# Kernel optimization log

Hardware: AMD Instinct MI355X
Metric: run time of the kernel (lower is better)

## Reference

```python
import math
import jax, jax.numpy as jnp
import numpy as np

N, C, H, W = 32, 64, 96, 96
SHIFT_H, SHIFT_W = 1, -1  # fixed values of the random roll shifts

def _dwconv(x, w, dilation, pad):
    # depthwise conv, x: (n,c,h,w), w: (c,1,kh,kw)
    return jax.lax.conv_general_dilated(
        x, w, window_strides=(1, 1), padding=((pad, pad), (pad, pad)),
        rhs_dilation=(dilation, dilation),
        dimension_numbers=('NCHW', 'OIHW', 'NCHW'),
        feature_group_count=x.shape[1])

def _unfold_1x7_d2(x):
    # F.unfold(x, (1,7), dilation=(1,2), padding=(0,6)) -> (n,c,7,h,w)
    n, c, h, w = x.shape
    xp = jnp.pad(x, ((0, 0), (0, 0), (0, 0), (6, 6)))
    return jnp.stack([xp[..., 2 * k: 2 * k + w] for k in range(7)], axis=2)

def setup_inputs() -> dict:
    key = jax.random.key(0)
    k0, k1, k2, k3, k4, k5 = jax.random.split(key, 6)
    std = 0.1
    return {
        'x':  jax.random.normal(k0, (N, C, H, W), dtype=jnp.float32),
        'w3': jax.random.normal(k1, (C, 1, 5, 5), dtype=jnp.float32) * std,
        'w4': jax.random.normal(k2, (C, 1, 3, 3), dtype=jnp.float32) * std,
        'p5': jax.random.normal(k3, (1, C, C), dtype=jnp.float32) * std,
        'p6': jax.random.normal(k4, (C, 1), dtype=jnp.float32) * std,
        'p8': jax.random.normal(k5, (C, C * 7), dtype=jnp.float32) * std,
    }

def reference(x, w3, w4, p5, p6, p8):
    n, c, h, w = x.shape
    hw = h * w
    t0 = x
    t1 = jnp.roll(jnp.roll(t0, SHIFT_H, axis=2), SHIFT_W, axis=3)
    # channel attention: (n,c,c)
    t2 = jnp.einsum('nci,ndi->ncd', t0.reshape(n, c, hw), t1.reshape(n, c, hw)) / math.sqrt(hw)
    t3 = _dwconv(t1, w3, dilation=1, pad=2)          # (n,c,h,w)
    t4 = _dwconv(t1, w4, dilation=2, pad=2)          # (n,c,h,w)
    t5 = p5 * t2                                      # (n,c,c)
    t6 = jnp.einsum('nchw,ce->nehw', t4, p6).reshape(n, h, w)
    t7 = _unfold_1x7_d2(t0).reshape(n, c * 7, hw)     # (n, c*7, hw)
    t8 = jnp.einsum('nbc,bd->ndc', t5, p8)            # (n, c*7, c)
    t9 = jnp.einsum('nci,ni->nc', t3.reshape(n, c, hw), t6.reshape(n, hw)) / math.sqrt(hw)
    t10 = jnp.einsum('nkc,nks->ncs', t8, t7) / math.sqrt(c * 7)  # (n,c,hw)
    t11 = t9[:, :, None] + t10
    return t11.reshape(n, c, h, w)
```

## Files before the change

### kernel.cpp

```cpp
#include <hip/hip_runtime.h>

#define NB 32
#define CCH 64
#define HH 96
#define WWID 96
#define HWP (HH*WWID)
#define K7 448

#define OFF_T5 4194304
#define OFF_T8 4325376
#define OFF_T6 4784128
#define OFF_T9 5079040

typedef __attribute__((ext_vector_type(8))) short short8;
typedef __attribute__((ext_vector_type(4))) short shortx4;
typedef __attribute__((ext_vector_type(4))) float floatx4;
typedef float __attribute__((ext_vector_type(4), aligned(4))) float4u;

__device__ __forceinline__ short f2bf(float x) {
    unsigned u = __float_as_uint(x);
    unsigned r = (u + 0x7FFF + ((u >> 16) & 1)) >> 16;
    return (short)r;
}

__device__ __forceinline__ void ld_ab(const float* __restrict__ xa, int base,
                                      float4u* va, float4u* vb, int t) {
#pragma unroll
    for (int i = 0; i < 2; i++) {
        int idx = i * 256 + t;
        int c = idx >> 3, k4 = idx & 7;
        int gi = base + k4 * 4;
        const float* xc = xa + c * HWP;
        va[i] = *(const float4u*)(xc + gi);
        int h = gi / WWID, w = gi - h * WWID;
        int hr = (h == 0) ? (HH - 1) : (h - 1);
        const float* xrow = xc + hr * WWID;
        if (w < 92) {
            vb[i] = *(const float4u*)(xrow + w + 1);
        } else {
            float4u tmp;
            tmp.x = xrow[93]; tmp.y = xrow[94]; tmp.z = xrow[95]; tmp.w = xrow[0];
            vb[i] = tmp;
        }
    }
}

__global__ __launch_bounds__(256) void k_t2(const float* __restrict__ x,
                                            float* __restrict__ t2p) {
    int blk = blockIdx.x;
    int n = blk >> 5, sl = blk & 31;
    int k0 = sl * 288;
    __shared__ short ash[2][64][40];
    __shared__ short bsh[2][64][40];
    int t = threadIdx.x;
    int lane = t & 63, wv = t >> 6;
    int q = lane >> 4, r16 = lane & 15;
    const float* xa = x + (size_t)n * CCH * HWP;

    floatx4 acc[4] = {};

    float4u va[2][2], vb[2][2];
    ld_ab(xa, k0,      va[0], vb[0], t);
    ld_ab(xa, k0 + 32, va[1], vb[1], t);

#pragma unroll
    for (int it = 0; it < 9; it++) {
        const int cur = it & 1;
#pragma unroll
        for (int i = 0; i < 2; i++) {
            int idx = i * 256 + t;
            int c = idx >> 3, k4 = idx & 7;
            shortx4 pa = {f2bf(va[cur][i].x), f2bf(va[cur][i].y),
                          f2bf(va[cur][i].z), f2bf(va[cur][i].w)};
            shortx4 pb = {f2bf(vb[cur][i].x), f2bf(vb[cur][i].y),
                          f2bf(vb[cur][i].z), f2bf(vb[cur][i].w)};
            *(shortx4*)&ash[cur][c][k4 * 4] = pa;
            *(shortx4*)&bsh[cur][c][k4 * 4] = pb;
        }
        if (it + 2 < 9)
            ld_ab(xa, k0 + (it + 2) * 32, va[cur], vb[cur], t);
        __syncthreads();
        short8 bfrag = *(const short8*)&bsh[cur][wv * 16 + r16][q * 8];
#pragma unroll
        for (int mi = 0; mi < 4; mi++) {
            short8 afrag = *(const short8*)&ash[cur][mi * 16 + r16][q * 8];
            acc[mi] = __builtin_amdgcn_mfma_f32_16x16x32_bf16(afrag, bfrag, acc[mi], 0, 0, 0);
        }
    }

    float* o = t2p + (size_t)(n * 32 + sl) * 4096;
#pragma unroll
    for (int mi = 0; mi < 4; mi++) {
        int m = mi * 16 + q * 4;
#pragma unroll
        for (int i = 0; i < 4; i++)
            o[(m + i) * 64 + wv * 16 + r16] = acc[mi][i];
    }
}

__global__ __launch_bounds__(256) void k_t5(const float* __restrict__ t2p,
                                            const float* __restrict__ p5,
                                            float* __restrict__ t5) {
    int idx = blockIdx.x * 256 + threadIdx.x;
    int n = idx >> 12, rc = idx & 4095;
    float s = 0.f;
#pragma unroll
    for (int sl = 0; sl < 32; sl++)
        s += t2p[((size_t)n * 32 + sl) * 4096 + rc];
    t5[idx] = s * p5[rc] * (1.0f / 96.0f);
}

__global__ __launch_bounds__(256) void k_t8(const float* __restrict__ t5,
                                            const float* __restrict__ p8,
                                            short* __restrict__ t8t) {
    int n = blockIdx.y;
    int idx = blockIdx.x * 256 + threadIdx.x;
    int k = idx >> 6, c = idx & 63;
    const float* t5n = t5 + (size_t)n * 4096;
    float s = 0.f;
#pragma unroll 8
    for (int b = 0; b < 64; b++)
        s += t5n[b * 64 + c] * p8[b * K7 + k];
    int c7 = k / 7, kk = k - c7 * 7;
    t8t[((size_t)n * 64 + c) * K7 + kk * 64 + c7] = f2bf(s * 0.04724555912f);
}

__global__ __launch_bounds__(256) void k_t6(const float* __restrict__ x,
                                            const float* __restrict__ w4,
                                            const float* __restrict__ p6,
                                            float* __restrict__ t6) {
    int n = blockIdx.y;
    int pix = blockIdx.x * 256 + threadIdx.x;
    int h = pix / WWID, w = pix - h * WWID;

    int off9[9];
    float m9[9];
#pragma unroll
    for (int i = 0; i < 3; i++) {
        int gh = h + (i - 1) * 2;
        bool vr = (gh >= 0) && (gh < HH);
        int srow = vr ? ((gh + HH - 1) % HH) * WWID : 0;
        float rm = vr ? 1.f : 0.f;
#pragma unroll
        for (int j = 0; j < 3; j++) {
            int gw = w + (j - 1) * 2;
            bool vc = (gw >= 0) && (gw < WWID);
            int scol = vc ? (gw + 1) % WWID : 0;
            off9[i * 3 + j] = srow + scol;
            m9[i * 3 + j] = vc ? rm : 0.f;
        }
    }
    const float* xn = x + (size_t)n * CCH * HWP;
    float acc = 0.f;
    for (int c = 0; c < CCH; c++) {
        const float* xc = xn + c * HWP;
        float pw = p6[c];
        const float* wc = w4 + c * 9;
#pragma unroll
        for (int ij = 0; ij < 9; ij++) {
            float wm = wc[ij] * pw * m9[ij];
            acc = fmaf(wm, xc[off9[ij]], acc);
        }
    }
    t6[(size_t)n * HWP + pix] = acc;
}

__global__ __launch_bounds__(256) void k_t9(const float* __restrict__ x,
                                            const float* __restrict__ w3,
                                            const float* __restrict__ t6,
                                            float* __restrict__ t9) {
    int n = blockIdx.y, c = blockIdx.x;
    __shared__ float xl[100][100];
    __shared__ float red[4];
    int t = threadIdx.x;
    const float* xc = x + ((size_t)n * CCH + c) * HWP;
    const float* t6n = t6 + (size_t)n * HWP;

    for (int idx = t; idx < 784; idx += 256) {
        if (idx < 400) {
            int r = idx / 100, col = idx - r * 100;
            int row = r < 2 ? r : r + 96;
            xl[row][col] = 0.f;
        } else {
            int rem = idx - 400;
            int h2 = rem >> 2, c4 = rem & 3;
            int col = c4 < 2 ? c4 : c4 + 96;
            xl[2 + h2][col] = 0.f;
        }
    }
    for (int idx = t; idx < HWP; idx += 256) {
        int h = idx / WWID, w = idx - h * WWID;
        int sh = (h == 0) ? (HH - 1) : (h - 1);
        int sw = (w == WWID - 1) ? 0 : (w + 1);
        xl[h + 2][w + 2] = xc[sh * WWID + sw];
    }
    float wv[25];
#pragma unroll
    for (int i = 0; i < 25; i++) wv[i] = w3[c * 25 + i];
    __syncthreads();

    float acc = 0.f;
#pragma unroll
    for (int g = 0; g < 9; g++) {
        int idx = g * 256 + t;
        int h = idx / 24, wg = idx - h * 24;
        int w0 = wg * 4;
        float4 tv = *(const float4*)(t6n + h * WWID + w0);
        float conv[4] = {0.f, 0.f, 0.f, 0.f};
#pragma unroll
        for (int kh = 0; kh < 5; kh++) {
            float4 ra = *(const float4*)&xl[h + kh][w0];
            float4 rb = *(const float4*)&xl[h + kh][w0 + 4];
            float r[8] = {ra.x, ra.y, ra.z, ra.w, rb.x, rb.y, rb.z, rb.w};
#pragma unroll
            for (int kw = 0; kw < 5; kw++) {
                float wk = wv[kh * 5 + kw];
                conv[0] = fmaf(wk, r[kw],     conv[0]);
                conv[1] = fmaf(wk, r[kw + 1], conv[1]);
                conv[2] = fmaf(wk, r[kw + 2], conv[2]);
                conv[3] = fmaf(wk, r[kw + 3], conv[3]);
            }
        }
        acc = fmaf(conv[0], tv.x, acc);
        acc = fmaf(conv[1], tv.y, acc);
        acc = fmaf(conv[2], tv.z, acc);
        acc = fmaf(conv[3], tv.w, acc);
    }
#pragma unroll
    for (int off = 32; off > 0; off >>= 1) acc += __shfl_down(acc, off, 64);
    if ((t & 63) == 0) red[t >> 6] = acc;
    __syncthreads();
    if (t == 0)
        t9[n * 64 + c] = (red[0] + red[1] + red[2] + red[3]) * (1.0f / 96.0f);
}

__global__ __launch_bounds__(256) void k_out(const float* __restrict__ x,
                                             const short* __restrict__ t8t,
                                             const float* __restrict__ t9,
                                             float* __restrict__ out) {
    int n = blockIdx.y;
    int h0 = blockIdx.x * 2;
    __shared__ short xsh[193 * 64];
    int t = threadIdx.x;

    if (t < 32) ((int*)xsh)[192 * 32 + t] = 0;

    const float* xn = x + (size_t)n * CCH * HWP;
#pragma unroll
    for (int i = 0; i < 12; i++) {
        int idx = i * 256 + t;
        int r = idx / 1536;
        int rem = idx - r * 1536;
        int c7g = rem / 96, w = rem - c7g * 96;
        const float* src = xn + (size_t)(c7g * 4) * HWP + (h0 + r) * WWID + w;
        shortx4 p = {f2bf(src[0]), f2bf(src[HWP]), f2bf(src[2 * HWP]), f2bf(src[3 * HWP])};
        int R = r * 96 + w;
        *(shortx4*)&xsh[R * 64 + ((c7g * 4) ^ ((R & 7) << 3))] = p;
    }
    __syncthreads();

    int lane = t & 63, wv = t >> 6;
    int q = lane >> 4, sl = lane & 15;
    int mh = wv & 1;
    int sh2 = wv >> 1;
    int rbase = sh2 * 96 - 6;
    floatx4 acc[2][6] = {};
    const short* Abase = t8t + (size_t)n * 64 * K7 + (mh * 32 + sl) * K7 + q * 8;

    auto computeB = [&](int kc, const short8* a) {
        int kk = kc >> 6;
        int c7b = (kc & 63) + q * 8;
        int iwb = sl + 2 * kk;
        short8 b[6];
#pragma unroll
        for (int sj = 0; sj < 6; sj++) {
            int iw = sj * 16 + iwb;
            int Rv;
            if (sj == 0)      Rv = (iw >= 6)  ? (rbase + iw) : 192;
            else if (sj == 5) Rv = (iw < 102) ? (rbase + iw) : 192;
            else              Rv = rbase + iw;
            b[sj] = *(const short8*)&xsh[Rv * 64 + (c7b ^ ((Rv & 7) << 3))];
        }
#pragma unroll
        for (int mi = 0; mi < 2; mi++)
#pragma unroll
            for (int sj = 0; sj < 6; sj++)
                acc[mi][sj] = __builtin_amdgcn_mfma_f32_16x16x32_bf16(
                    a[mi], b[sj], acc[mi][sj], 0, 0, 0);
    };

    short8 a0[2], a1[2];
    a0[0] = *(const short8*)(Abase);
    a0[1] = *(const short8*)(Abase + 16 * K7);

    for (int kc = 0; kc < K7; kc += 64) {
        a1[0] = *(const short8*)(Abase + kc + 32);
        a1[1] = *(const short8*)(Abase + 16 * K7 + kc + 32);
        computeB(kc, a0);
        if (kc + 64 < K7) {
            a0[0] = *(const short8*)(Abase + kc + 64);
            a0[1] = *(const short8*)(Abase + 16 * K7 + kc + 64);
        }
        computeB(kc + 32, a1);
    }

    const float* t9n = t9 + n * 64;
#pragma unroll
    for (int mi = 0; mi < 2; mi++) {
#pragma unroll
        for (int i = 0; i < 4; i++) {
            int c = (mh * 2 + mi) * 16 + q * 4 + i;
            float tv = t9n[c];
            float* orow = out + ((size_t)n * CCH + c) * HWP + (h0 + sh2) * WWID;
#pragma unroll
            for (int sj = 0; sj < 6; sj++)
                orow[sj * 16 + sl] = acc[mi][sj][i] + tv;
        }
    }
}

extern "C" void kernel_launch(void* const* d_in, const int* in_sizes, int n_in,
                              void* d_out, int out_size, void* d_ws, size_t ws_size,
                              hipStream_t stream) {
    const float* x  = (const float*)d_in[0];
    const float* w3 = (const float*)d_in[1];
    const float* w4 = (const float*)d_in[2];
    const float* p5 = (const float*)d_in[3];
    const float* p6 = (const float*)d_in[4];
    const float* p8 = (const float*)d_in[5];
    float* out = (float*)d_out;
    float* ws  = (float*)d_ws;

    float* t2p = ws;
    float* t5  = ws + OFF_T5;
    short* t8t = (short*)(ws + OFF_T8);
    float* t6  = ws + OFF_T6;
    float* t9  = ws + OFF_T9;

    k_t2<<<1024, 256, 0, stream>>>(x, t2p);
    k_t5<<<512, 256, 0, stream>>>(t2p, p5, t5);
    k_t8<<<dim3(112, 32), 256, 0, stream>>>(t5, p8, t8t);
    k_t6<<<dim3(36, 32), 256, 0, stream>>>(x, w4, p6, t6);
    k_t9<<<dim3(64, 32), 256, 0, stream>>>(x, w3, t6, t9);
    k_out<<<dim3(48, 32), 256, 0, stream>>>(x, t8t, t9, out);
}
```

Baseline: 268.1 us.

## Software-pipeline k_out over three row pairs with double-buffered LDS

Each k_out block now handles six rows (three row pairs) instead of two. It prefetches the next pair of x rows into registers while MFMAs run on the current LDS buffer, then converts them and stores to the alternate buffer. The goal is to hide global-load latency behind compute and to amortise per-block setup such as the t9 loads. In exchange LDS use doubles, register pressure rises from the 48-float prefetch array, and the grid shrinks to 512 blocks, which may reduce occupancy and parallelism on a 256-CU device.

```diff
diff --git a/kernel.cpp b/kernel.cpp
--- a/kernel.cpp
+++ b/kernel.cpp
@@ -239,82 +239,123 @@
                                              const float* __restrict__ t9,
                                              float* __restrict__ out) {
     int n = blockIdx.y;
-    int h0 = blockIdx.x * 2;
-    __shared__ short xsh[193 * 64];
+    int hg = blockIdx.x;
+    __shared__ short xsh[2][193 * 64];
     int t = threadIdx.x;
 
-    if (t < 32) ((int*)xsh)[192 * 32 + t] = 0;
+    if (t < 32) {
+        ((int*)xsh[0])[192 * 32 + t] = 0;
+        ((int*)xsh[1])[192 * 32 + t] = 0;
+    }
 
     const float* xn = x + (size_t)n * CCH * HWP;
+    int lane = t & 63, wv = t >> 6;
+    int q = lane >> 4, sl = lane & 15;
+    int mh = wv & 1;
+    int sh2 = wv >> 1;
+    int rbase = sh2 * 96 - 6;
+    const short* Abase = t8t + (size_t)n * 64 * K7 + (mh * 32 + sl) * K7 + q * 8;
+
+    float tvv[2][4];
+#pragma unroll
+    for (int mi = 0; mi < 2; mi++)
+#pragma unroll
+        for (int i = 0; i < 4; i++)
+            tvv[mi][i] = t9[n * 64 + (mh * 2 + mi) * 16 + q * 4 + i];
+
+    float pf[12][4];
+
 #pragma unroll
     for (int i = 0; i < 12; i++) {
         int idx = i * 256 + t;
         int r = idx / 1536;
         int rem = idx - r * 1536;
         int c7g = rem / 96, w = rem - c7g * 96;
-        const float* src = xn + (size_t)(c7g * 4) * HWP + (h0 + r) * WWID + w;
-        shortx4 p = {f2bf(src[0]), f2bf(src[HWP]), f2bf(src[2 * HWP]), f2bf(src[3 * HWP])};
+        const float* src = xn + (size_t)(c7g * 4) * HWP + (hg * 6 + r) * WWID + w;
+        pf[i][0] = src[0]; pf[i][1] = src[HWP];
+        pf[i][2] = src[2 * HWP]; pf[i][3] = src[3 * HWP];
+    }
+#pragma unroll
+    for (int i = 0; i < 12; i++) {
+        int idx = i * 256 + t;
+        int r = idx / 1536;
+        int rem = idx - r * 1536;
+        int c7g = rem / 96, w = rem - c7g * 96;
         int R = r * 96 + w;
-        *(shortx4*)&xsh[R * 64 + ((c7g * 4) ^ ((R & 7) << 3))] = p;
+        shortx4 pk = {f2bf(pf[i][0]), f2bf(pf[i][1]), f2bf(pf[i][2]), f2bf(pf[i][3])};
+        *(shortx4*)&xsh[0][R * 64 + ((c7g * 4) ^ ((R & 7) << 3))] = pk;
     }
     __syncthreads();
 
-    int lane = t & 63, wv = t >> 6;
-    int q = lane >> 4, sl = lane & 15;
-    int mh = wv & 1;
-    int sh2 = wv >> 1;
-    int rbase = sh2 * 96 - 6;
-    floatx4 acc[2][6] = {};
-    const short* Abase = t8t + (size_t)n * 64 * K7 + (mh * 32 + sl) * K7 + q * 8;
-
-    auto computeB = [&](int kc, const short8* a) {
-        int kk = kc >> 6;
-        int c7b = (kc & 63) + q * 8;
-        int iwb = sl + 2 * kk;
-        short8 b[6];
-#pragma unroll
-        for (int sj = 0; sj < 6; sj++) {
-            int iw = sj * 16 + iwb;
-            int Rv;
-            if (sj == 0)      Rv = (iw >= 6)  ? (rbase + iw) : 192;
-            else if (sj == 5) Rv = (iw < 102) ? (rbase + iw) : 192;
-            else              Rv = rbase + iw;
-            b[sj] = *(const short8*)&xsh[Rv * 64 + (c7b ^ ((Rv & 7) << 3))];
-        }
-#pragma unroll
-        for (int mi = 0; mi < 2; mi++)
-#pragma unroll
-            for (int sj = 0; sj < 6; sj++)
-                acc[mi][sj] = __builtin_amdgcn_mfma_f32_16x16x32_bf16(
-                    a[mi], b[sj], acc[mi][sj], 0, 0, 0);
-    };
-
-    short8 a0[2], a1[2];
-    a0[0] = *(const short8*)(Abase);
-    a0[1] = *(const short8*)(Abase + 16 * K7);
-
-    for (int kc = 0; kc < K7; kc += 64) {
-        a1[0] = *(const short8*)(Abase + kc + 32);
-        a1[1] = *(const short8*)(Abase + 16 * K7 + kc + 32);
-        computeB(kc, a0);
-        if (kc + 64 < K7) {
-            a0[0] = *(const short8*)(Abase + kc + 64);
-            a0[1] = *(const short8*)(Abase + 16 * K7 + kc + 64);
-        }
-        computeB(kc + 32, a1);
-    }
-
-    const float* t9n = t9 + n * 64;
-#pragma unroll
-    for (int mi = 0; mi < 2; mi++) {
-#pragma unroll
-        for (int i = 0; i < 4; i++) {
-            int c = (mh * 2 + mi) * 16 + q * 4 + i;
-            float tv = t9n[c];
-            float* orow = out + ((size_t)n * CCH + c) * HWP + (h0 + sh2) * WWID;
-#pragma unroll
-            for (int sj = 0; sj < 6; sj++)
-                orow[sj * 16 + sl] = acc[mi][sj][i] + tv;
+#pragma unroll
+    for (int p = 0; p < 3; p++) {
+        if (p < 2) {
+#pragma unroll
+            for (int i = 0; i < 12; i++) {
+                int idx = i * 256 + t;
+                int r = idx / 1536;
+                int rem = idx - r * 1536;
+                int c7g = rem / 96, w = rem - c7g * 96;
+                const float* src = xn + (size_t)(c7g * 4) * HWP
+                                      + (hg * 6 + (p + 1) * 2 + r) * WWID + w;
+                pf[i][0] = src[0]; pf[i][1] = src[HWP];
+                pf[i][2] = src[2 * HWP]; pf[i][3] = src[3 * HWP];
+            }
+        }
+
+        const short* Bb = xsh[p & 1];
+        floatx4 acc[2][6] = {};
+        for (int kc = 0; kc < K7; kc += 32) {
+            int kk = kc >> 6;
+            int c7b = (kc & 63) + q * 8;
+            int iwb = sl + 2 * kk;
+            short8 a[2], b[6];
+#pragma unroll
+            for (int mi = 0; mi < 2; mi++)
+                a[mi] = *(const short8*)(Abase + mi * 16 * K7 + kc);
+#pragma unroll
+            for (int sj = 0; sj < 6; sj++) {
+                int iw = sj * 16 + iwb;
+                int Rv;
+                if (sj == 0)      Rv = (iw >= 6)  ? (rbase + iw) : 192;
+                else if (sj == 5) Rv = (iw < 102) ? (rbase + iw) : 192;
+                else              Rv = rbase + iw;
+                b[sj] = *(const short8*)&Bb[Rv * 64 + (c7b ^ ((Rv & 7) << 3))];
+            }
+#pragma unroll
+            for (int mi = 0; mi < 2; mi++)
+#pragma unroll
+                for (int sj = 0; sj < 6; sj++)
+                    acc[mi][sj] = __builtin_amdgcn_mfma_f32_16x16x32_bf16(
+                        a[mi], b[sj], acc[mi][sj], 0, 0, 0);
+        }
+
+        int h0p = hg * 6 + p * 2;
+#pragma unroll
+        for (int mi = 0; mi < 2; mi++) {
+#pragma unroll
+            for (int i = 0; i < 4; i++) {
+                int c = (mh * 2 + mi) * 16 + q * 4 + i;
+                float* orow = out + ((size_t)n * CCH + c) * HWP + (h0p + sh2) * WWID;
+#pragma unroll
+                for (int sj = 0; sj < 6; sj++)
+                    orow[sj * 16 + sl] = acc[mi][sj][i] + tvv[mi][i];
+            }
+        }
+
+        if (p < 2) {
+#pragma unroll
+            for (int i = 0; i < 12; i++) {
+                int idx = i * 256 + t;
+                int r = idx / 1536;
+                int rem = idx - r * 1536;
+                int c7g = rem / 96, w = rem - c7g * 96;
+                int R = r * 96 + w;
+                shortx4 pk = {f2bf(pf[i][0]), f2bf(pf[i][1]),
+                              f2bf(pf[i][2]), f2bf(pf[i][3])};
+                *(shortx4*)&xsh[(p + 1) & 1][R * 64 + ((c7g * 4) ^ ((R & 7) << 3))] = pk;
+            }
+            __syncthreads();
         }
     }
 }
@@ -342,5 +383,5 @@
     k_t8<<<dim3(112, 32), 256, 0, stream>>>(t5, p8, t8t);
     k_t6<<<dim3(36, 32), 256, 0, stream>>>(x, w4, p6, t6);
     k_t9<<<dim3(64, 32), 256, 0, stream>>>(x, w3, t6, t9);
-    k_out<<<dim3(48, 32), 256, 0, stream>>>(x, t8t, t9, out);
-}
+    k_out<<<dim3(16, 32), 256, 0, stream>>>(x, t8t, t9, out);
+}
```

Result: no change. 270.9 us (+1.1%).
